# Kernel optimization log

Hardware: AMD Instinct MI355X
Metric: run time of the kernel (lower is better)

Reference implementation:

```python
import jax, jax.numpy as jnp
import numpy as np
from math import sqrt


def setup_inputs() -> dict:
    key = jax.random.key(0)
    k1, k2, k3 = jax.random.split(key, 3)
    B, L, H, E = 2, 2048, 16, 64
    queries = jax.random.normal(k1, (B, L, H, E), dtype=jnp.float32)
    keys = jax.random.normal(k2, (B, L, H, E), dtype=jnp.float32)
    values = jax.random.normal(k3, (B, L, H, E), dtype=jnp.float32)
    return {"queries": queries, "keys": keys, "values": values}


def reference(queries, keys, values):
    # queries: [B,L,H,E], keys: [B,S,H,E], values: [B,S,H,D]
    B, L, H, E = queries.shape
    S = keys.shape[1]
    scale = 1.0 / sqrt(E)
    # raw scores [B,H,L,S]
    scores = jnp.einsum('blhe,bshe->bhls', queries, keys)
    # triangular causal mask (True above diagonal -> masked)
    causal = jnp.triu(jnp.ones((L, S), dtype=bool), k=1)  # [L,S]
    scores = jnp.where(causal[None, None, :, :], -jnp.inf, scores)
    A = jax.nn.softmax(scale * scores, axis=-1)  # dropout p=0 -> identity
    V = jnp.einsum('bhls,bshd->blhd', A, values)
    return V
```

## Files before the change

kernel.cpp:

```cpp
#include <hip/hip_runtime.h>

typedef __attribute__((ext_vector_type(2))) __fp16 fp16x2;
typedef __attribute__((ext_vector_type(4))) _Float16 half4;
typedef __attribute__((ext_vector_type(8))) _Float16 half8;
typedef __attribute__((ext_vector_type(4))) float floatx4;

typedef union { half8 h8; half4 h4[2]; } h8split;

#define B_SZ  2
#define L_SEQ 2048
#define NH    16
#define EDIM  64
#define LOG2E 1.4426950408889634f
#define QSCALE (0.125f * LOG2E)

__device__ __forceinline__ int swz(int s, int ch) {
    return ch ^ (((s & 7) + 2 * (s >> 4)) & 7);
}

__global__ __launch_bounds__(256, 1)
void convert_kv(const float* __restrict__ K, const float* __restrict__ V,
                _Float16* __restrict__ Kh, _Float16* __restrict__ Vt)
{
    __shared__ __align__(16) _Float16 Tile[64 * 64];
    const int st = blockIdx.x & 31;
    const int h  = (blockIdx.x >> 5) & 15;
    const int b  = blockIdx.x >> 9;
    const int s0 = st * 64;
    const int t  = threadIdx.x;
    const int r  = t >> 2, c = t & 3;
    const size_t bh   = (size_t)b * NH + h;
    const size_t src  = (((size_t)b * L_SEQ + s0 + r) * NH + h) * EDIM + c * 16;
    const size_t cbase = bh * (size_t)(L_SEQ * EDIM) + (size_t)st * 4096;

    {
        const float4* kp = (const float4*)(K + src);
        float4 f[4];
#pragma unroll
        for (int i = 0; i < 4; ++i) f[i] = kp[i];
        _Float16 tmp[16];
#pragma unroll
        for (int i = 0; i < 4; ++i) {
            fp16x2 a  = __builtin_amdgcn_cvt_pkrtz(f[i].x, f[i].y);
            fp16x2 b2 = __builtin_amdgcn_cvt_pkrtz(f[i].z, f[i].w);
            tmp[4*i+0] = (_Float16)a[0];  tmp[4*i+1] = (_Float16)a[1];
            tmp[4*i+2] = (_Float16)b2[0]; tmp[4*i+3] = (_Float16)b2[1];
        }
        _Float16* kd = Kh + cbase + (size_t)(r >> 4) * 1024 + (c >> 1) * 512 + (r & 15) * 8;
        *(half8*)(kd + (((2 * c)     & 3) * 128)) = *(half8*)&tmp[0];
        *(half8*)(kd + (((2 * c + 1) & 3) * 128)) = *(half8*)&tmp[8];
    }
    {
        const float4* vp = (const float4*)(V + src);
        float4 f[4];
#pragma unroll
        for (int i = 0; i < 4; ++i) f[i] = vp[i];
        _Float16 tmp[16];
#pragma unroll
        for (int i = 0; i < 4; ++i) {
            fp16x2 a  = __builtin_amdgcn_cvt_pkrtz(f[i].x, f[i].y);
            fp16x2 b2 = __builtin_amdgcn_cvt_pkrtz(f[i].z, f[i].w);
            tmp[4*i+0] = (_Float16)a[0];  tmp[4*i+1] = (_Float16)a[1];
            tmp[4*i+2] = (_Float16)b2[0]; tmp[4*i+3] = (_Float16)b2[1];
        }
        _Float16* base = &Tile[r * 64];
        *(half8*)(base + swz(r, 2 * c)     * 8) = *(half8*)&tmp[0];
        *(half8*)(base + swz(r, 2 * c + 1) * 8) = *(half8*)&tmp[8];
    }
    __syncthreads();
    {
        const int d = t >> 2, seg = t & 3;
        _Float16 tmp[16];
#pragma unroll
        for (int i = 0; i < 16; ++i) {
            const int s = seg * 16 + i;
            tmp[i] = Tile[s * 64 + swz(s, d >> 3) * 8 + (d & 7)];
        }
        _Float16* vd = Vt + cbase + (size_t)seg * 1024 + (d & 15) * 16 + (d >> 4) * 4;
#pragma unroll
        for (int kg = 0; kg < 4; ++kg)
            *(half4*)(vd + kg * 256) = *(half4*)&tmp[kg * 4];
    }
}

__global__ __launch_bounds__(256, 4)
void fa_fwd(const float* __restrict__ Q, const _Float16* __restrict__ Kh,
            const _Float16* __restrict__ Vt, float* __restrict__ O)
{
    __shared__ float slabL[4][4][17];
    __shared__ __align__(16) float slabO[4][16][68];
    __shared__ __align__(16) _Float16 Qs[64 * 64];

    const int i  = blockIdx.x;
    const int bh = i & 31;
    const int v  = i >> 5;
    const int u  = v & 7, j = v >> 3;
    const int tile = (j == 0) ? (31 - u) : (j == 1) ? u : (j == 2) ? (23 - u) : (8 + u);
    const int b    = bh >> 4;
    const int h    = bh & 15;
    const int w    = threadIdx.x >> 6;
    const int lane = threadIdx.x & 63;
    const int ln16 = lane & 15;
    const int quad = lane >> 4;
    const int qrow0 = tile * 64;
    const int nch   = tile + 1;

    {
        const int t = threadIdx.x;
        const int r = t >> 2, c = t & 3;
        const float4* qp = (const float4*)(Q + (((size_t)b * L_SEQ + qrow0 + r) * NH + h) * EDIM + c * 16);
        float4 f[4];
#pragma unroll
        for (int k = 0; k < 4; ++k) f[k] = qp[k];
        _Float16 tmp[16];
#pragma unroll
        for (int k = 0; k < 4; ++k) {
            fp16x2 a  = __builtin_amdgcn_cvt_pkrtz(f[k].x * QSCALE, f[k].y * QSCALE);
            fp16x2 b2 = __builtin_amdgcn_cvt_pkrtz(f[k].z * QSCALE, f[k].w * QSCALE);
            tmp[4*k+0] = (_Float16)a[0];  tmp[4*k+1] = (_Float16)a[1];
            tmp[4*k+2] = (_Float16)b2[0]; tmp[4*k+3] = (_Float16)b2[1];
        }
        const int key = (r & 7) << 3;
        _Float16* qd = Qs + r * 64;
        *(half8*)(qd + ((c * 16)     ^ key)) = *(half8*)&tmp[0];
        *(half8*)(qd + ((c * 16 + 8) ^ key)) = *(half8*)&tmp[8];
    }
    __syncthreads();

    const int qkey  = (ln16 & 7) << 3;
    const int baseA = ln16 * 64 + ((quad * 8) ^ qkey);
    const int baseB = ln16 * 64 + ((32 + quad * 8) ^ qkey);

    floatx4 acc[4][4];
#pragma unroll
    for (int dt = 0; dt < 4; ++dt)
#pragma unroll
        for (int g = 0; g < 4; ++g) acc[dt][g] = (floatx4){0.f,0.f,0.f,0.f};
    float lp[4] = {0.f, 0.f, 0.f, 0.f};

    const _Float16* kb = Kh + (size_t)bh * (L_SEQ * EDIM) + w * 1024 + lane * 8;
    const _Float16* vb = Vt + (size_t)bh * (L_SEQ * EDIM) + w * 1024 + lane * 16;

    half8 k0c = *(const half8*)kb;
    half8 k1c = *(const half8*)(kb + 512);
    half8 v01c = *(const half8*)vb;
    half8 v23c = *(const half8*)(vb + 8);

    for (int it = 0; it < nch; ++it) {
        const bool masked = (it == nch - 1);
        const half8 ka  = k0c;
        const half8 kb2 = k1c;
        h8split u01, u23;
        u01.h8 = v01c;
        u23.h8 = v23c;
        const half4 vc0 = u01.h4[0];
        const half4 vc1 = u01.h4[1];
        const half4 vc2 = u23.h4[0];
        const half4 vc3 = u23.h4[1];

#pragma unroll
        for (int g = 0; g < 4; ++g) {
            half8 qa = *(const half8*)(Qs + baseA + g * 1024);
            half8 qb = *(const half8*)(Qs + baseB + g * 1024);
            floatx4 z = (floatx4){0.f,0.f,0.f,0.f};
            z = __builtin_amdgcn_mfma_f32_16x16x32_f16(ka, qa, z, 0, 0, 0);
            floatx4 st = __builtin_amdgcn_mfma_f32_16x16x32_f16(kb2, qb, z, 0, 0, 0);

            if (g == 0 && it + 1 < nch) {
                const _Float16* kp = kb + (size_t)(it + 1) * 4096;
                k0c = *(const half8*)kp;
                k1c = *(const half8*)(kp + 512);
            }
            if (g == 1 && it + 1 < nch) {
                const _Float16* vp = vb + (size_t)(it + 1) * 4096;
                v01c = *(const half8*)vp;
                v23c = *(const half8*)(vp + 8);
            }

            float p[4];
#pragma unroll
            for (int r = 0; r < 4; ++r) {
                float e = __builtin_amdgcn_exp2f(st[r]);
                if (masked) {
                    const int keyi = it * 64 + w * 16 + quad * 4 + r;
                    e = (keyi <= qrow0 + g * 16 + ln16) ? e : 0.0f;
                }
                p[r] = e;
            }
            lp[g] += (p[0] + p[1]) + (p[2] + p[3]);
            fp16x2 lo = __builtin_amdgcn_cvt_pkrtz(p[0], p[1]);
            fp16x2 hi = __builtin_amdgcn_cvt_pkrtz(p[2], p[3]);
            half4 pf;
            pf[0] = (_Float16)lo[0]; pf[1] = (_Float16)lo[1];
            pf[2] = (_Float16)hi[0]; pf[3] = (_Float16)hi[1];

            acc[0][g] = __builtin_amdgcn_mfma_f32_16x16x16f16(vc0, pf, acc[0][g], 0, 0, 0);
            acc[1][g] = __builtin_amdgcn_mfma_f32_16x16x16f16(vc1, pf, acc[1][g], 0, 0, 0);
            acc[2][g] = __builtin_amdgcn_mfma_f32_16x16x16f16(vc2, pf, acc[2][g], 0, 0, 0);
            acc[3][g] = __builtin_amdgcn_mfma_f32_16x16x16f16(vc3, pf, acc[3][g], 0, 0, 0);
        }
    }

#pragma unroll
    for (int g = 0; g < 4; ++g) {
        lp[g] += __shfl_xor(lp[g], 16);
        lp[g] += __shfl_xor(lp[g], 32);
    }
    if (quad == 0) {
#pragma unroll
        for (int g = 0; g < 4; ++g) slabL[w][g][ln16] = lp[g];
    }

    const int q   = threadIdx.x >> 2;
    const int seg = threadIdx.x & 3;
    float inv = 0.f;
#pragma unroll
    for (int dt = 0; dt < 4; ++dt) {
#pragma unroll
        for (int g = 0; g < 4; ++g)
#pragma unroll
            for (int r = 0; r < 4; ++r)
                slabO[w][quad * 4 + r][g * 16 + ln16] = acc[dt][g][r];
        __syncthreads();
        if (dt == 0) {
            float lt = slabL[0][q >> 4][q & 15] + slabL[1][q >> 4][q & 15]
                     + slabL[2][q >> 4][q & 15] + slabL[3][q >> 4][q & 15];
            inv = 1.0f / lt;
        }
        float o0 = 0.f, o1 = 0.f, o2 = 0.f, o3 = 0.f;
#pragma unroll
        for (int ww = 0; ww < 4; ++ww) {
            o0 += slabO[ww][seg * 4 + 0][q];
            o1 += slabO[ww][seg * 4 + 1][q];
            o2 += slabO[ww][seg * 4 + 2][q];
            o3 += slabO[ww][seg * 4 + 3][q];
        }
        float4 ov = {o0 * inv, o1 * inv, o2 * inv, o3 * inv};
        *(float4*)(O + (((size_t)b * L_SEQ + qrow0 + q) * NH + h) * EDIM + dt * 16 + seg * 4) = ov;
        if (dt < 3) __syncthreads();
    }
}

extern "C" void kernel_launch(void* const* d_in, const int* in_sizes, int n_in,
                              void* d_out, int out_size, void* d_ws, size_t ws_size,
                              hipStream_t stream) {
    const float* Q = (const float*)d_in[0];
    const float* K = (const float*)d_in[1];
    const float* V = (const float*)d_in[2];
    float* O = (float*)d_out;
    _Float16* Kh = (_Float16*)d_ws;
    _Float16* Vt = Kh + (size_t)B_SZ * NH * L_SEQ * EDIM;
    convert_kv<<<dim3(B_SZ * NH * (L_SEQ / 64)), dim3(256), 0, stream>>>(K, V, Kh, Vt);
    fa_fwd<<<dim3(32 * 32), dim3(256), 0, stream>>>(Q, Kh, Vt, O);
}
```

Baseline: 140.8 us.

## Split work by query rows per wave with LDS double-buffered K/V tiles

Each wave now owns 16 query rows and keeps its Q fragments in registers, where before each wave owned a slice of keys and all four waves shared the Q tile. K and V chunks are staged through double-buffered shared memory so all waves read the same tile, and the V-transpose layout in the conversion kernel changes to match. This removes the cross-wave reduction of partial outputs and row sums at the end, along with its shared-memory slabs and barriers. The cost is a block barrier on every key chunk, plus extra LDS reads of K and V per wave.

```diff
diff --git a/kernel.cpp b/kernel.cpp
--- a/kernel.cpp
+++ b/kernel.cpp
@@ -76,10 +76,11 @@
             const int s = seg * 16 + i;
             tmp[i] = Tile[s * 64 + swz(s, d >> 3) * 8 + (d & 7)];
         }
-        _Float16* vd = Vt + cbase + (size_t)seg * 1024 + (d & 15) * 16 + (d >> 4) * 4;
+        _Float16* vd = Vt + cbase + (size_t)seg * 1024 + (d >> 5) * 512
+                       + (d & 15) * 8 + ((d >> 4) & 1) * 4;
 #pragma unroll
         for (int kg = 0; kg < 4; ++kg)
-            *(half4*)(vd + kg * 256) = *(half4*)&tmp[kg * 4];
+            *(half4*)(vd + kg * 128) = *(half4*)&tmp[kg * 4];
     }
 }
 
@@ -87,9 +88,8 @@
 void fa_fwd(const float* __restrict__ Q, const _Float16* __restrict__ Kh,
             const _Float16* __restrict__ Vt, float* __restrict__ O)
 {
-    __shared__ float slabL[4][4][17];
-    __shared__ __align__(16) float slabO[4][16][68];
-    __shared__ __align__(16) _Float16 Qs[64 * 64];
+    __shared__ __align__(16) _Float16 Kb[2][4096];
+    __shared__ __align__(16) _Float16 Vb[2][4096];
 
     const int i  = blockIdx.x;
     const int bh = i & 31;
@@ -98,146 +98,127 @@
     const int tile = (j == 0) ? (31 - u) : (j == 1) ? u : (j == 2) ? (23 - u) : (8 + u);
     const int b    = bh >> 4;
     const int h    = bh & 15;
-    const int w    = threadIdx.x >> 6;
+    const int wid  = threadIdx.x >> 6;
     const int lane = threadIdx.x & 63;
     const int ln16 = lane & 15;
     const int quad = lane >> 4;
     const int qrow0 = tile * 64;
     const int nch   = tile + 1;
-
-    {
-        const int t = threadIdx.x;
-        const int r = t >> 2, c = t & 3;
-        const float4* qp = (const float4*)(Q + (((size_t)b * L_SEQ + qrow0 + r) * NH + h) * EDIM + c * 16);
-        float4 f[4];
-#pragma unroll
-        for (int k = 0; k < 4; ++k) f[k] = qp[k];
-        _Float16 tmp[16];
-#pragma unroll
-        for (int k = 0; k < 4; ++k) {
-            fp16x2 a  = __builtin_amdgcn_cvt_pkrtz(f[k].x * QSCALE, f[k].y * QSCALE);
-            fp16x2 b2 = __builtin_amdgcn_cvt_pkrtz(f[k].z * QSCALE, f[k].w * QSCALE);
-            tmp[4*k+0] = (_Float16)a[0];  tmp[4*k+1] = (_Float16)a[1];
-            tmp[4*k+2] = (_Float16)b2[0]; tmp[4*k+3] = (_Float16)b2[1];
-        }
-        const int key = (r & 7) << 3;
-        _Float16* qd = Qs + r * 64;
-        *(half8*)(qd + ((c * 16)     ^ key)) = *(half8*)&tmp[0];
-        *(half8*)(qd + ((c * 16 + 8) ^ key)) = *(half8*)&tmp[8];
+    const int t16   = threadIdx.x * 16;
+    const int lane8 = lane * 8;
+
+    half8 qfA, qfB;
+    {
+        const float4* qp = (const float4*)(Q + (((size_t)b * L_SEQ + qrow0 + wid * 16 + ln16) * NH + h) * EDIM + quad * 8);
+        float4 f0 = qp[0], f1 = qp[1];
+        float4 f2 = qp[8], f3 = qp[9];
+        fp16x2 t0 = __builtin_amdgcn_cvt_pkrtz(f0.x * QSCALE, f0.y * QSCALE);
+        fp16x2 t1 = __builtin_amdgcn_cvt_pkrtz(f0.z * QSCALE, f0.w * QSCALE);
+        fp16x2 t2 = __builtin_amdgcn_cvt_pkrtz(f1.x * QSCALE, f1.y * QSCALE);
+        fp16x2 t3 = __builtin_amdgcn_cvt_pkrtz(f1.z * QSCALE, f1.w * QSCALE);
+        qfA[0] = (_Float16)t0[0]; qfA[1] = (_Float16)t0[1];
+        qfA[2] = (_Float16)t1[0]; qfA[3] = (_Float16)t1[1];
+        qfA[4] = (_Float16)t2[0]; qfA[5] = (_Float16)t2[1];
+        qfA[6] = (_Float16)t3[0]; qfA[7] = (_Float16)t3[1];
+        t0 = __builtin_amdgcn_cvt_pkrtz(f2.x * QSCALE, f2.y * QSCALE);
+        t1 = __builtin_amdgcn_cvt_pkrtz(f2.z * QSCALE, f2.w * QSCALE);
+        t2 = __builtin_amdgcn_cvt_pkrtz(f3.x * QSCALE, f3.y * QSCALE);
+        t3 = __builtin_amdgcn_cvt_pkrtz(f3.z * QSCALE, f3.w * QSCALE);
+        qfB[0] = (_Float16)t0[0]; qfB[1] = (_Float16)t0[1];
+        qfB[2] = (_Float16)t1[0]; qfB[3] = (_Float16)t1[1];
+        qfB[4] = (_Float16)t2[0]; qfB[5] = (_Float16)t2[1];
+        qfB[6] = (_Float16)t3[0]; qfB[7] = (_Float16)t3[1];
+    }
+
+    const char* kgb = (const char*)(Kh + (size_t)bh * (L_SEQ * EDIM));
+    const char* vgb = (const char*)(Vt + (size_t)bh * (L_SEQ * EDIM));
+
+    {
+        half8 ka = *(const half8*)(kgb + t16);
+        half8 kc = *(const half8*)(kgb + 4096 + t16);
+        half8 va = *(const half8*)(vgb + t16);
+        half8 vc = *(const half8*)(vgb + 4096 + t16);
+        *(half8*)((char*)Kb[0] + t16)        = ka;
+        *(half8*)((char*)Kb[0] + 4096 + t16) = kc;
+        *(half8*)((char*)Vb[0] + t16)        = va;
+        *(half8*)((char*)Vb[0] + 4096 + t16) = vc;
     }
     __syncthreads();
 
-    const int qkey  = (ln16 & 7) << 3;
-    const int baseA = ln16 * 64 + ((quad * 8) ^ qkey);
-    const int baseB = ln16 * 64 + ((32 + quad * 8) ^ qkey);
-
-    floatx4 acc[4][4];
-#pragma unroll
-    for (int dt = 0; dt < 4; ++dt)
-#pragma unroll
-        for (int g = 0; g < 4; ++g) acc[dt][g] = (floatx4){0.f,0.f,0.f,0.f};
-    float lp[4] = {0.f, 0.f, 0.f, 0.f};
-
-    const _Float16* kb = Kh + (size_t)bh * (L_SEQ * EDIM) + w * 1024 + lane * 8;
-    const _Float16* vb = Vt + (size_t)bh * (L_SEQ * EDIM) + w * 1024 + lane * 16;
-
-    half8 k0c = *(const half8*)kb;
-    half8 k1c = *(const half8*)(kb + 512);
-    half8 v01c = *(const half8*)vb;
-    half8 v23c = *(const half8*)(vb + 8);
+    floatx4 acc[4];
+#pragma unroll
+    for (int dt = 0; dt < 4; ++dt) acc[dt] = (floatx4){0.f, 0.f, 0.f, 0.f};
+    float lp = 0.f;
 
     for (int it = 0; it < nch; ++it) {
+        const bool last = (it + 1 >= nch);
+        half8 ka, kc2, va, vc2;
+        if (!last) {
+            const char* ks = kgb + (size_t)(it + 1) * 8192;
+            const char* vs = vgb + (size_t)(it + 1) * 8192;
+            ka  = *(const half8*)(ks + t16);
+            kc2 = *(const half8*)(ks + 4096 + t16);
+            va  = *(const half8*)(vs + t16);
+            vc2 = *(const half8*)(vs + 4096 + t16);
+        }
+
+        const _Float16* kc = Kb[it & 1];
+        const _Float16* vv = Vb[it & 1];
         const bool masked = (it == nch - 1);
-        const half8 ka  = k0c;
-        const half8 kb2 = k1c;
-        h8split u01, u23;
-        u01.h8 = v01c;
-        u23.h8 = v23c;
-        const half4 vc0 = u01.h4[0];
-        const half4 vc1 = u01.h4[1];
-        const half4 vc2 = u23.h4[0];
-        const half4 vc3 = u23.h4[1];
-
-#pragma unroll
-        for (int g = 0; g < 4; ++g) {
-            half8 qa = *(const half8*)(Qs + baseA + g * 1024);
-            half8 qb = *(const half8*)(Qs + baseB + g * 1024);
-            floatx4 z = (floatx4){0.f,0.f,0.f,0.f};
-            z = __builtin_amdgcn_mfma_f32_16x16x32_f16(ka, qa, z, 0, 0, 0);
-            floatx4 st = __builtin_amdgcn_mfma_f32_16x16x32_f16(kb2, qb, z, 0, 0, 0);
-
-            if (g == 0 && it + 1 < nch) {
-                const _Float16* kp = kb + (size_t)(it + 1) * 4096;
-                k0c = *(const half8*)kp;
-                k1c = *(const half8*)(kp + 512);
-            }
-            if (g == 1 && it + 1 < nch) {
-                const _Float16* vp = vb + (size_t)(it + 1) * 4096;
-                v01c = *(const half8*)vp;
-                v23c = *(const half8*)(vp + 8);
-            }
+#pragma unroll
+        for (int s = 0; s < 4; ++s) {
+            half8 k0 = *(const half8*)(kc + s * 1024 + lane8);
+            half8 k1 = *(const half8*)(kc + s * 1024 + 512 + lane8);
+            floatx4 z = (floatx4){0.f, 0.f, 0.f, 0.f};
+            z = __builtin_amdgcn_mfma_f32_16x16x32_f16(k0, qfA, z, 0, 0, 0);
+            floatx4 st = __builtin_amdgcn_mfma_f32_16x16x32_f16(k1, qfB, z, 0, 0, 0);
 
             float p[4];
 #pragma unroll
             for (int r = 0; r < 4; ++r) {
                 float e = __builtin_amdgcn_exp2f(st[r]);
                 if (masked) {
-                    const int keyi = it * 64 + w * 16 + quad * 4 + r;
-                    e = (keyi <= qrow0 + g * 16 + ln16) ? e : 0.0f;
+                    const int key = it * 64 + s * 16 + quad * 4 + r;
+                    e = (key <= qrow0 + wid * 16 + ln16) ? e : 0.0f;
                 }
                 p[r] = e;
             }
-            lp[g] += (p[0] + p[1]) + (p[2] + p[3]);
+            lp += (p[0] + p[1]) + (p[2] + p[3]);
             fp16x2 lo = __builtin_amdgcn_cvt_pkrtz(p[0], p[1]);
             fp16x2 hi = __builtin_amdgcn_cvt_pkrtz(p[2], p[3]);
             half4 pf;
             pf[0] = (_Float16)lo[0]; pf[1] = (_Float16)lo[1];
             pf[2] = (_Float16)hi[0]; pf[3] = (_Float16)hi[1];
 
-            acc[0][g] = __builtin_amdgcn_mfma_f32_16x16x16f16(vc0, pf, acc[0][g], 0, 0, 0);
-            acc[1][g] = __builtin_amdgcn_mfma_f32_16x16x16f16(vc1, pf, acc[1][g], 0, 0, 0);
-            acc[2][g] = __builtin_amdgcn_mfma_f32_16x16x16f16(vc2, pf, acc[2][g], 0, 0, 0);
-            acc[3][g] = __builtin_amdgcn_mfma_f32_16x16x16f16(vc3, pf, acc[3][g], 0, 0, 0);
-        }
-    }
-
-#pragma unroll
-    for (int g = 0; g < 4; ++g) {
-        lp[g] += __shfl_xor(lp[g], 16);
-        lp[g] += __shfl_xor(lp[g], 32);
-    }
-    if (quad == 0) {
-#pragma unroll
-        for (int g = 0; g < 4; ++g) slabL[w][g][ln16] = lp[g];
-    }
-
-    const int q   = threadIdx.x >> 2;
-    const int seg = threadIdx.x & 3;
-    float inv = 0.f;
+            h8split u01, u23;
+            u01.h8 = *(const half8*)(vv + s * 1024 + lane8);
+            u23.h8 = *(const half8*)(vv + s * 1024 + 512 + lane8);
+            acc[0] = __builtin_amdgcn_mfma_f32_16x16x16f16(u01.h4[0], pf, acc[0], 0, 0, 0);
+            acc[1] = __builtin_amdgcn_mfma_f32_16x16x16f16(u01.h4[1], pf, acc[1], 0, 0, 0);
+            acc[2] = __builtin_amdgcn_mfma_f32_16x16x16f16(u23.h4[0], pf, acc[2], 0, 0, 0);
+            acc[3] = __builtin_amdgcn_mfma_f32_16x16x16f16(u23.h4[1], pf, acc[3], 0, 0, 0);
+        }
+
+        if (!last) {
+            char* kd = (char*)Kb[(it + 1) & 1];
+            char* vd = (char*)Vb[(it + 1) & 1];
+            *(half8*)(kd + t16)        = ka;
+            *(half8*)(kd + 4096 + t16) = kc2;
+            *(half8*)(vd + t16)        = va;
+            *(half8*)(vd + 4096 + t16) = vc2;
+            __syncthreads();
+        }
+    }
+
+    lp += __shfl_xor(lp, 16);
+    lp += __shfl_xor(lp, 32);
+    const float inv = 1.0f / lp;
+    float* op = O + (((size_t)b * L_SEQ + qrow0 + wid * 16 + ln16) * NH + h) * EDIM;
 #pragma unroll
     for (int dt = 0; dt < 4; ++dt) {
-#pragma unroll
-        for (int g = 0; g < 4; ++g)
-#pragma unroll
-            for (int r = 0; r < 4; ++r)
-                slabO[w][quad * 4 + r][g * 16 + ln16] = acc[dt][g][r];
-        __syncthreads();
-        if (dt == 0) {
-            float lt = slabL[0][q >> 4][q & 15] + slabL[1][q >> 4][q & 15]
-                     + slabL[2][q >> 4][q & 15] + slabL[3][q >> 4][q & 15];
-            inv = 1.0f / lt;
-        }
-        float o0 = 0.f, o1 = 0.f, o2 = 0.f, o3 = 0.f;
-#pragma unroll
-        for (int ww = 0; ww < 4; ++ww) {
-            o0 += slabO[ww][seg * 4 + 0][q];
-            o1 += slabO[ww][seg * 4 + 1][q];
-            o2 += slabO[ww][seg * 4 + 2][q];
-            o3 += slabO[ww][seg * 4 + 3][q];
-        }
-        float4 ov = {o0 * inv, o1 * inv, o2 * inv, o3 * inv};
-        *(float4*)(O + (((size_t)b * L_SEQ + qrow0 + q) * NH + h) * EDIM + dt * 16 + seg * 4) = ov;
-        if (dt < 3) __syncthreads();
+        float4 ov = {acc[dt][0] * inv, acc[dt][1] * inv,
+                     acc[dt][2] * inv, acc[dt][3] * inv};
+        *(float4*)(op + dt * 16 + quad * 4) = ov;
     }
 }
 
```

Result: faster. 118.9 us (-15.6%).
